# Kernel optimization log

Measured on AMD Instinct MI355X. Metric: run time of the kernel, lower is better.

## Reference

```python
import jax, jax.numpy as jnp
import numpy as np

N = 2560          # 64 graphs * 40 nodes (hard-coded by view(64,40,40))
E = 163840        # edges, avg degree 64
HEADS = 4
IN_C = 32
H0 = 128          # hidden_dims[0] per head
H1 = 128          # hidden_dims[1] per head
OUT_E = 40
EPS_BN = 1e-5


def _glorot(key, shape):
    fan = sum(shape[-2:]) if len(shape) > 1 else shape[0]
    return jax.random.normal(key, shape, dtype=jnp.float32) * (2.0 / fan) ** 0.5


def setup_inputs() -> dict:
    key = jax.random.key(0)
    ks = jax.random.split(key, 24)
    inp = {
        "x": jax.random.normal(ks[0], (N, IN_C), dtype=jnp.float32),
        "edge_index": jax.random.randint(ks[1], (2, E), 0, N, dtype=jnp.int32),
        "pos": jax.random.normal(ks[2], (N, 2), dtype=jnp.float32),
        "mask": jax.random.randint(ks[3], (N,), 0, 2, dtype=jnp.int32),
        "adjacency": jax.random.uniform(ks[4], (N, OUT_E), dtype=jnp.float32),
        # GAT layer 1 (in -> heads*H0)
        "W1": _glorot(ks[5], (IN_C, HEADS * H0)),
        "att_src1": _glorot(ks[6], (HEADS, H0)),
        "att_dst1": _glorot(ks[7], (HEADS, H0)),
        "We1": _glorot(ks[8], (1, HEADS * H0)),
        "att_e1": _glorot(ks[9], (HEADS, H0)),
        "bias1": jnp.zeros((HEADS * H0,), dtype=jnp.float32),
        # BatchNorm 1
        "g1": jnp.ones((HEADS * H0,), dtype=jnp.float32),
        "be1": jnp.zeros((HEADS * H0,), dtype=jnp.float32),
        # GAT layer 2 (heads*H0 -> heads*H1)
        "W2": _glorot(ks[10], (HEADS * H0, HEADS * H1)),
        "att_src2": _glorot(ks[11], (HEADS, H1)),
        "att_dst2": _glorot(ks[12], (HEADS, H1)),
        "We2": _glorot(ks[13], (1, HEADS * H1)),
        "att_e2": _glorot(ks[14], (HEADS, H1)),
        "bias2": jnp.zeros((HEADS * H1,), dtype=jnp.float32),
        # BatchNorm 2
        "g2": jnp.ones((HEADS * H1,), dtype=jnp.float32),
        "be2": jnp.zeros((HEADS * H1,), dtype=jnp.float32),
        # fc_edge
        "Wfc": _glorot(ks[15], (HEADS * H1, OUT_E)),
        "bfc": jnp.zeros((OUT_E,), dtype=jnp.float32),
    }
    return inp


def _gat(x, src, dst, ew, W, att_s, att_d, We, att_e, bias, heads, c):
    # x: [N, Fin] -> h: [N, H, C]
    h = (x @ W).reshape(-1, heads, c)
    a_s = (h * att_s).sum(-1)                       # [N, H]
    a_d = (h * att_d).sum(-1)                       # [N, H]
    he = (ew[:, None] @ We).reshape(-1, heads, c)   # [E, H, C] edge attr proj
    a_e = (he * att_e).sum(-1)                      # [E, H]
    alpha = jax.nn.leaky_relu(a_s[src] + a_d[dst] + a_e, 0.2)
    # segment softmax over destination nodes
    m = jax.ops.segment_max(alpha, dst, num_segments=N)
    alpha = jnp.exp(alpha - m[dst])
    denom = jax.ops.segment_sum(alpha, dst, num_segments=N)
    alpha = alpha / (denom[dst] + 1e-16)
    out = jax.ops.segment_sum(h[src] * alpha[:, :, None], dst, num_segments=N)
    return out.reshape(-1, heads * c) + bias


def _batchnorm(x, g, b):
    mu = x.mean(0)
    var = x.var(0)
    return (x - mu) * jax.lax.rsqrt(var + EPS_BN) * g + b


def reference(x, edge_index, pos, mask, adjacency,
              W1, att_src1, att_dst1, We1, att_e1, bias1, g1, be1,
              W2, att_src2, att_dst2, We2, att_e2, bias2, g2, be2,
              Wfc, bfc):
    src, dst = edge_index[0], edge_index[1]
    ew = 1.0 / (jnp.linalg.norm(pos[src] - pos[dst], axis=1) + 1e-6)  # [E]

    h = _gat(x, src, dst, ew, W1, att_src1, att_dst1, We1, att_e1, bias1, HEADS, H0)
    h = jax.nn.relu(_batchnorm(h, g1, be1))

    e = _gat(h, src, dst, ew, W2, att_src2, att_dst2, We2, att_e2, bias2, HEADS, H1)
    e = jax.nn.relu(_batchnorm(e, g2, be2))

    out_edge = e @ Wfc + bfc                     # [N, 40]
    out_edge = out_edge * mask[:, None].astype(out_edge.dtype)
    out_edge = out_edge.reshape(64, 40, 40)
    return out_edge + adjacency.reshape(64, 40, 40)
```

## Files before the change

### kernel.cpp

```cpp
#include <hip/hip_runtime.h>
#include <hip/hip_bf16.h>

#define NN 2560
#define NE 163840
#define NH 4
#define NC 128
#define NF 512
#define OUTE 40
#define CSTR 256

typedef short bf16x8 __attribute__((ext_vector_type(8)));
typedef float f32x4 __attribute__((ext_vector_type(4)));

__device__ inline ushort f2bf(float f) {
    uint u = __float_as_uint(f);
    uint r = u + 0x7FFF + ((u >> 16) & 1);
    return (ushort)(r >> 16);
}
__device__ inline float bflo(uint v) { return __uint_as_float(v << 16); }
__device__ inline float bfhi(uint v) { return __uint_as_float(v & 0xFFFF0000u); }
__device__ inline float bf2f(ushort u) { return __uint_as_float(((uint)u) << 16); }
__device__ inline float rdlanef(float v, int l) {
    return __int_as_float(__builtin_amdgcn_readlane(__float_as_int(v), l));
}
__device__ inline int rdlanei(int v, int l) {
    return __builtin_amdgcn_readlane(v, l);
}
__device__ inline float sel4(float r0, float r1, float r2, float r3, int hd) {
    return (hd & 2) ? ((hd & 1) ? r3 : r2) : ((hd & 1) ? r1 : r0);
}

__global__ __launch_bounds__(256) void k_csr_gemm1(const int* __restrict__ ei,
        const float* __restrict__ pos, int* __restrict__ deg,
        int2* __restrict__ csrp, int* __restrict__ ovf_cnt, int4* __restrict__ ovf,
        const float* __restrict__ We1, const float* __restrict__ ae1,
        const float* __restrict__ We2, const float* __restrict__ ae2,
        float* __restrict__ dote,
        const float* __restrict__ Wfc, ushort* __restrict__ WfcT,
        const float* __restrict__ W2, ushort* __restrict__ W2T,
        const float* __restrict__ x, const float* __restrict__ W1,
        const float* __restrict__ atts, const float* __restrict__ attd,
        ushort* __restrict__ hb, float* __restrict__ as_, float* __restrict__ ad_) {
    __shared__ ushort tile[64][72];
    __shared__ float s_x[4][32];
    __shared__ float4 s_red[4][4];
    int b = blockIdx.x;
    if (b < 640) {
        int e = b * 256 + threadIdx.x;
        int s = ei[e], d = ei[NE + e];
        float dx = pos[2 * s] - pos[2 * d];
        float dy = pos[2 * s + 1] - pos[2 * d + 1];
        float w = 1.0f / (sqrtf(dx * dx + dy * dy) + 1e-6f);
        int r = atomicAdd(&deg[d], 1);
        if (r < CSTR) {
            csrp[(d << 8) + r] = make_int2(s, __float_as_int(w));
        } else {
            int i = atomicAdd(ovf_cnt, 1);
            ovf[i] = make_int4(d, s, __float_as_int(w), 0);
        }
        return;
    }
    if (b < 642) {
        int t = threadIdx.x;
        const float* W = (b == 641) ? We2 : We1;
        const float* A = (b == 641) ? ae2 : ae1;
        int w = t >> 6, l = t & 63;
        float p = W[w * 128 + l] * A[w * 128 + l] + W[w * 128 + 64 + l] * A[w * 128 + 64 + l];
#pragma unroll
        for (int o = 32; o > 0; o >>= 1) p += __shfl_down(p, o);
        if (l == 0) dote[(b - 640) * 4 + w] = p;
        return;
    }
    if (b < 738) {
        int idx = (b - 642) * 256 + threadIdx.x;
        int j = idx >> 9, k = idx & 511;
        WfcT[idx] = (j < OUTE) ? f2bf(Wfc[k * OUTE + j]) : (ushort)0;
        return;
    }
    if (b < 802) {
        int id = b - 738;
        int n0 = (id & 7) * 64, k0 = (id >> 3) * 64;
        int t = threadIdx.x;
        int r = t >> 2, cseg = (t & 3) * 16;
#pragma unroll
        for (int c = 0; c < 16; c += 4) {
            float4 v = *(const float4*)&W2[(k0 + r) * 512 + n0 + cseg + c];
            tile[cseg + c + 0][r] = f2bf(v.x);
            tile[cseg + c + 1][r] = f2bf(v.y);
            tile[cseg + c + 2][r] = f2bf(v.z);
            tile[cseg + c + 3][r] = f2bf(v.w);
        }
        __syncthreads();
        *(uint4*)&W2T[(n0 + r) * 512 + k0 + cseg]     = *(uint4*)&tile[r][cseg];
        *(uint4*)&W2T[(n0 + r) * 512 + k0 + cseg + 8] = *(uint4*)&tile[r][cseg + 8];
        return;
    }
    int n0 = (b - 802) * 4, t = threadIdx.x;
    if (t < 128) s_x[t >> 5][t & 31] = x[n0 * 32 + t];
    __syncthreads();
    float a0[4] = {0.f, 0.f, 0.f, 0.f}, a1[4] = {0.f, 0.f, 0.f, 0.f};
#pragma unroll
    for (int k = 0; k < 32; k++) {
        float w0 = W1[k * 512 + t];
        float w1 = W1[k * 512 + t + 256];
#pragma unroll
        for (int nn = 0; nn < 4; nn++) {
            a0[nn] += s_x[nn][k] * w0;
            a1[nn] += s_x[nn][k] * w1;
        }
    }
    float sa0 = atts[t], sa1 = atts[t + 256];
    float da0 = attd[t], da1 = attd[t + 256];
    int w = t >> 6, lane = t & 63;
#pragma unroll
    for (int nn = 0; nn < 4; nn++) {
        hb[(n0 + nn) * 512 + t] = f2bf(a0[nn]);
        hb[(n0 + nn) * 512 + t + 256] = f2bf(a1[nn]);
        float ps0 = a0[nn] * sa0, pd0 = a0[nn] * da0;
        float ps1 = a1[nn] * sa1, pd1 = a1[nn] * da1;
#pragma unroll
        for (int o = 32; o > 0; o >>= 1) {
            ps0 += __shfl_xor(ps0, o); pd0 += __shfl_xor(pd0, o);
            ps1 += __shfl_xor(ps1, o); pd1 += __shfl_xor(pd1, o);
        }
        if (lane == 0) s_red[w][nn] = make_float4(ps0, pd0, ps1, pd1);
    }
    __syncthreads();
    if (t < 4) {
        int nn = t, n = n0 + nn;
        float4 r0 = s_red[0][nn], r1 = s_red[1][nn], r2 = s_red[2][nn], r3 = s_red[3][nn];
        as_[n * 4 + 0] = r0.x + r1.x; as_[n * 4 + 1] = r2.x + r3.x;
        as_[n * 4 + 2] = r0.z + r1.z; as_[n * 4 + 3] = r2.z + r3.z;
        ad_[n * 4 + 0] = r0.y + r1.y; ad_[n * 4 + 1] = r2.y + r3.y;
        ad_[n * 4 + 2] = r0.w + r1.w; ad_[n * 4 + 3] = r2.w + r3.w;
    }
}

__global__ __launch_bounds__(128) void k_edge_agg(const int* __restrict__ deg_,
        const int2* __restrict__ csrp, const int* __restrict__ ovf_cnt,
        const int4* __restrict__ ovf, const float* __restrict__ as_,
        const float* __restrict__ ad_, const float* __restrict__ dote,
        const ushort* __restrict__ hb, const float* __restrict__ bias,
        ushort* __restrict__ outb) {
    int w = threadIdx.x >> 6, lane = threadIdx.x & 63;
    int n = blockIdx.x * 2 + w;
    int beg = n << 8;
    int degn = deg_[n];
    int dmain = min(degn, CSTR);
    float4 adv = *(const float4*)&ad_[n * 4];
    float4 dv  = *(const float4*)dote;
    float La0 = -1e30f, La1 = -1e30f, La2 = -1e30f, La3 = -1e30f;
    float Lb0 = -1e30f, Lb1 = -1e30f, Lb2 = -1e30f, Lb3 = -1e30f;
    int off0 = 0, off1 = 0;
    if (lane < dmain) {
        int2 p = csrp[beg + lane];
        off0 = p.x * NF;
        float4 a = *(const float4*)&as_[p.x * 4];
        float ww = __int_as_float(p.y);
        float v0 = a.x + adv.x + ww * dv.x; La0 = v0 > 0.f ? v0 : 0.2f * v0;
        float v1 = a.y + adv.y + ww * dv.y; La1 = v1 > 0.f ? v1 : 0.2f * v1;
        float v2 = a.z + adv.z + ww * dv.z; La2 = v2 > 0.f ? v2 : 0.2f * v2;
        float v3 = a.w + adv.w + ww * dv.w; La3 = v3 > 0.f ? v3 : 0.2f * v3;
    }
    if (lane + 64 < dmain) {
        int2 p = csrp[beg + lane + 64];
        off1 = p.x * NF;
        float4 a = *(const float4*)&as_[p.x * 4];
        float ww = __int_as_float(p.y);
        float v0 = a.x + adv.x + ww * dv.x; Lb0 = v0 > 0.f ? v0 : 0.2f * v0;
        float v1 = a.y + adv.y + ww * dv.y; Lb1 = v1 > 0.f ? v1 : 0.2f * v1;
        float v2 = a.z + adv.z + ww * dv.z; Lb2 = v2 > 0.f ? v2 : 0.2f * v2;
        float v3 = a.w + adv.w + ww * dv.w; Lb3 = v3 > 0.f ? v3 : 0.2f * v3;
    }
    float mx0 = fmaxf(La0, Lb0), mx1 = fmaxf(La1, Lb1);
    float mx2 = fmaxf(La2, Lb2), mx3 = fmaxf(La3, Lb3);
    for (int e = 128 + lane; e < dmain; e += 64) {
        int2 p = csrp[beg + e];
        float4 a = *(const float4*)&as_[p.x * 4];
        float ww = __int_as_float(p.y);
        float v0 = a.x + adv.x + ww * dv.x; v0 = v0 > 0.f ? v0 : 0.2f * v0;
        float v1 = a.y + adv.y + ww * dv.y; v1 = v1 > 0.f ? v1 : 0.2f * v1;
        float v2 = a.z + adv.z + ww * dv.z; v2 = v2 > 0.f ? v2 : 0.2f * v2;
        float v3 = a.w + adv.w + ww * dv.w; v3 = v3 > 0.f ? v3 : 0.2f * v3;
        mx0 = fmaxf(mx0, v0); mx1 = fmaxf(mx1, v1);
        mx2 = fmaxf(mx2, v2); mx3 = fmaxf(mx3, v3);
    }
    if (degn > CSTR) {
        int oc = *ovf_cnt;
        for (int i = lane; i < oc; i += 64) {
            int4 o = ovf[i];
            if (o.x == n) {
                float4 a = *(const float4*)&as_[o.y * 4];
                float ww = __int_as_float(o.z);
                float v0 = a.x + adv.x + ww * dv.x; v0 = v0 > 0.f ? v0 : 0.2f * v0;
                float v1 = a.y + adv.y + ww * dv.y; v1 = v1 > 0.f ? v1 : 0.2f * v1;
                float v2 = a.z + adv.z + ww * dv.z; v2 = v2 > 0.f ? v2 : 0.2f * v2;
                float v3 = a.w + adv.w + ww * dv.w; v3 = v3 > 0.f ? v3 : 0.2f * v3;
                mx0 = fmaxf(mx0, v0); mx1 = fmaxf(mx1, v1);
                mx2 = fmaxf(mx2, v2); mx3 = fmaxf(mx3, v3);
            }
        }
    }
#pragma unroll
    for (int o = 32; o > 0; o >>= 1) {
        mx0 = fmaxf(mx0, __shfl_xor(mx0, o));
        mx1 = fmaxf(mx1, __shfl_xor(mx1, o));
        mx2 = fmaxf(mx2, __shfl_xor(mx2, o));
        mx3 = fmaxf(mx3, __shfl_xor(mx3, o));
    }
    float Aa0 = __expf(La0 - mx0), Aa1 = __expf(La1 - mx1);
    float Aa2 = __expf(La2 - mx2), Aa3 = __expf(La3 - mx3);
    float Ab0 = __expf(Lb0 - mx0), Ab1 = __expf(Lb1 - mx1);
    float Ab2 = __expf(Lb2 - mx2), Ab3 = __expf(Lb3 - mx3);
    float s0 = Aa0 + Ab0, s1 = Aa1 + Ab1, s2 = Aa2 + Ab2, s3 = Aa3 + Ab3;
    for (int e = 128 + lane; e < dmain; e += 64) {
        int2 p = csrp[beg + e];
        float4 a = *(const float4*)&as_[p.x * 4];
        float ww = __int_as_float(p.y);
        float v0 = a.x + adv.x + ww * dv.x; v0 = v0 > 0.f ? v0 : 0.2f * v0;
        float v1 = a.y + adv.y + ww * dv.y; v1 = v1 > 0.f ? v1 : 0.2f * v1;
        float v2 = a.z + adv.z + ww * dv.z; v2 = v2 > 0.f ? v2 : 0.2f * v2;
        float v3 = a.w + adv.w + ww * dv.w; v3 = v3 > 0.f ? v3 : 0.2f * v3;
        s0 += __expf(v0 - mx0); s1 += __expf(v1 - mx1);
        s2 += __expf(v2 - mx2); s3 += __expf(v3 - mx3);
    }
    if (degn > CSTR) {
        int oc = *ovf_cnt;
        for (int i = lane; i < oc; i += 64) {
            int4 o = ovf[i];
            if (o.x == n) {
                float4 a = *(const float4*)&as_[o.y * 4];
                float ww = __int_as_float(o.z);
                float v0 = a.x + adv.x + ww * dv.x; v0 = v0 > 0.f ? v0 : 0.2f * v0;
                float v1 = a.y + adv.y + ww * dv.y; v1 = v1 > 0.f ? v1 : 0.2f * v1;
                float v2 = a.z + adv.z + ww * dv.z; v2 = v2 > 0.f ? v2 : 0.2f * v2;
                float v3 = a.w + adv.w + ww * dv.w; v3 = v3 > 0.f ? v3 : 0.2f * v3;
                s0 += __expf(v0 - mx0); s1 += __expf(v1 - mx1);
                s2 += __expf(v2 - mx2); s3 += __expf(v3 - mx3);
            }
        }
    }
#pragma unroll
    for (int o = 32; o > 0; o >>= 1) {
        s0 += __shfl_xor(s0, o); s1 += __shfl_xor(s1, o);
        s2 += __shfl_xor(s2, o); s3 += __shfl_xor(s3, o);
    }
    float inv0 = 1.f / (s0 + 1e-16f), inv1 = 1.f / (s1 + 1e-16f);
    float inv2 = 1.f / (s2 + 1e-16f), inv3 = 1.f / (s3 + 1e-16f);
    int hd = lane >> 4;
    const ushort* hbase = hb + 8 * lane;
    float acc0 = 0.f, acc1 = 0.f, acc2 = 0.f, acc3 = 0.f;
    float acc4 = 0.f, acc5 = 0.f, acc6 = 0.f, acc7 = 0.f;
    int m0 = min(dmain, 64);
#pragma unroll 16
    for (int e = 0; e < m0; e++) {
        float r0 = rdlanef(Aa0, e), r1 = rdlanef(Aa1, e);
        float r2 = rdlanef(Aa2, e), r3 = rdlanef(Aa3, e);
        float a = sel4(r0, r1, r2, r3, hd);
        int o = rdlanei(off0, e);
        uint4 v = *(const uint4*)(hbase + o);
        acc0 += a * bflo(v.x); acc1 += a * bfhi(v.x);
        acc2 += a * bflo(v.y); acc3 += a * bfhi(v.y);
        acc4 += a * bflo(v.z); acc5 += a * bfhi(v.z);
        acc6 += a * bflo(v.w); acc7 += a * bfhi(v.w);
    }
    int m1 = min(dmain, 128);
#pragma unroll 16
    for (int e = 64; e < m1; e++) {
        float r0 = rdlanef(Ab0, e - 64), r1 = rdlanef(Ab1, e - 64);
        float r2 = rdlanef(Ab2, e - 64), r3 = rdlanef(Ab3, e - 64);
        float a = sel4(r0, r1, r2, r3, hd);
        int o = rdlanei(off1, e - 64);
        uint4 v = *(const uint4*)(hbase + o);
        acc0 += a * bflo(v.x); acc1 += a * bfhi(v.x);
        acc2 += a * bflo(v.y); acc3 += a * bfhi(v.y);
        acc4 += a * bflo(v.z); acc5 += a * bfhi(v.z);
        acc6 += a * bflo(v.w); acc7 += a * bfhi(v.w);
    }
    float adh = sel4(adv.x, adv.y, adv.z, adv.w, hd);
    float dh  = sel4(dv.x, dv.y, dv.z, dv.w, hd);
    float mxh = sel4(mx0, mx1, mx2, mx3, hd);
    float ash;
    for (int e = 128; e < dmain; e++) {
        int2 p = csrp[beg + e];
        ash = as_[p.x * 4 + hd];
        float ww = __int_as_float(p.y);
        float vv = ash + adh + ww * dh; vv = vv > 0.f ? vv : 0.2f * vv;
        float a = __expf(vv - mxh);
        uint4 v = *(const uint4*)(hbase + p.x * NF);
        acc0 += a * bflo(v.x); acc1 += a * bfhi(v.x);
        acc2 += a * bflo(v.y); acc3 += a * bfhi(v.y);
        acc4 += a * bflo(v.z); acc5 += a * bfhi(v.z);
        acc6 += a * bflo(v.w); acc7 += a * bfhi(v.w);
    }
    if (degn > CSTR) {
        int oc = *ovf_cnt;
        for (int i = 0; i < oc; i++) {
            int4 o = ovf[i];
            if (o.x == n) {
                ash = as_[o.y * 4 + hd];
                float ww = __int_as_float(o.z);
                float vv = ash + adh + ww * dh; vv = vv > 0.f ? vv : 0.2f * vv;
                float a = __expf(vv - mxh);
                uint4 v = *(const uint4*)(hbase + o.y * NF);
                acc0 += a * bflo(v.x); acc1 += a * bfhi(v.x);
                acc2 += a * bflo(v.y); acc3 += a * bfhi(v.y);
                acc4 += a * bflo(v.z); acc5 += a * bfhi(v.z);
                acc6 += a * bflo(v.w); acc7 += a * bfhi(v.w);
            }
        }
    }
    float invh = sel4(inv0, inv1, inv2, inv3, hd);
    int ch = 8 * lane;
    float4 b0 = *(const float4*)&bias[ch];
    float4 b1 = *(const float4*)&bias[ch + 4];
    uint4 ov;
    ov.x = (uint)f2bf(acc0 * invh + b0.x) | ((uint)f2bf(acc1 * invh + b0.y) << 16);
    ov.y = (uint)f2bf(acc2 * invh + b0.z) | ((uint)f2bf(acc3 * invh + b0.w) << 16);
    ov.z = (uint)f2bf(acc4 * invh + b1.x) | ((uint)f2bf(acc5 * invh + b1.y) << 16);
    ov.w = (uint)f2bf(acc6 * invh + b1.z) | ((uint)f2bf(acc7 * invh + b1.w) << 16);
    *(uint4*)&outb[n * NF + ch] = ov;
}

__global__ __launch_bounds__(256) void k_bnstats(const ushort* __restrict__ xs,
        float* __restrict__ stats) {
    __shared__ float ps[2048];
    __shared__ float pq[2048];
    int t = threadIdx.x;
    int c8 = (t & 63) * 8, rr = t >> 6;
    float s[8] = {0.f,0.f,0.f,0.f,0.f,0.f,0.f,0.f};
    float q[8] = {0.f,0.f,0.f,0.f,0.f,0.f,0.f,0.f};
#pragma unroll
    for (int rj = 0; rj < 4; rj++) {
        int r = blockIdx.x * 16 + rr * 4 + rj;
        uint4 v = *(const uint4*)&xs[r * NF + c8];
        float vv[8];
        vv[0] = bflo(v.x); vv[1] = bfhi(v.x); vv[2] = bflo(v.y); vv[3] = bfhi(v.y);
        vv[4] = bflo(v.z); vv[5] = bfhi(v.z); vv[6] = bflo(v.w); vv[7] = bfhi(v.w);
#pragma unroll
        for (int c = 0; c < 8; c++) { s[c] += vv[c]; q[c] += vv[c] * vv[c]; }
    }
#pragma unroll
    for (int c = 0; c < 8; c++) {
        ps[rr * 512 + c8 + c] = s[c];
        pq[rr * 512 + c8 + c] = q[c];
    }
    __syncthreads();
    for (int ch = t; ch < 512; ch += 256) {
        atomicAdd(&stats[ch], ps[ch] + ps[512 + ch] + ps[1024 + ch] + ps[1536 + ch]);
        atomicAdd(&stats[NF + ch], pq[ch] + pq[512 + ch] + pq[1024 + ch] + pq[1536 + ch]);
    }
}

__global__ __launch_bounds__(256) void k_gemm2_bn_att(const ushort* __restrict__ Ab,
        const float* __restrict__ stats, const float* __restrict__ g,
        const float* __restrict__ bb, const ushort* __restrict__ BT,
        const float* __restrict__ atts, const float* __restrict__ attd,
        ushort* __restrict__ Cb, float* __restrict__ as_, float* __restrict__ ad_) {
    __shared__ ushort As[64][40];
    __shared__ ushort Bs[128][40];
    __shared__ float s_scale[512], s_shift[512];
    __shared__ float s_ps[2][64], s_pd[2][64];
    int t = threadIdx.x;
    const float invn = 1.0f / (float)NN;
    {
        int j = t;
#pragma unroll
        for (int rep = 0; rep < 2; rep++, j += 256) {
            float mu = stats[j] * invn;
            float var = stats[NF + j] * invn - mu * mu;
            float sc = rsqrtf(var + 1e-5f) * g[j];
            s_scale[j] = sc;
            s_shift[j] = bb[j] - mu * sc;
        }
    }
    int head = blockIdx.x;
    int rowBase = blockIdx.y * 64, colBase = head * 128;
    int w = t >> 6, lane = t & 63;
    int wm = (w >> 1) * 32, wn = (w & 1) * 64;
    int lm = lane & 15, q = lane >> 4;
    f32x4 acc[2][4] = {};
    int sr2 = t >> 2, sk = (t & 3) * 8;
    for (int k0 = 0; k0 < 512; k0 += 32) {
        __syncthreads();
        int jb = k0 + sk;
        float sc[8], sh[8];
#pragma unroll
        for (int c = 0; c < 8; c++) { sc[c] = s_scale[jb + c]; sh[c] = s_shift[jb + c]; }
        uint4 a8 = *(const uint4*)&Ab[(rowBase + sr2) * 512 + jb];
        uint4 b0 = *(const uint4*)&BT[(colBase + sr2) * 512 + jb];
        uint4 b1 = *(const uint4*)&BT[(colBase + 64 + sr2) * 512 + jb];
        ushort pa0[8];
        float av[8];
        av[0] = bflo(a8.x); av[1] = bfhi(a8.x); av[2] = bflo(a8.y); av[3] = bfhi(a8.y);
        av[4] = bflo(a8.z); av[5] = bfhi(a8.z); av[6] = bflo(a8.w); av[7] = bfhi(a8.w);
#pragma unroll
        for (int c = 0; c < 8; c++)
            pa0[c] = f2bf(fmaxf(av[c] * sc[c] + sh[c], 0.f));
        *(uint4*)&As[sr2][sk]      = *(uint4*)pa0;
        *(uint4*)&Bs[sr2][sk]      = b0;
        *(uint4*)&Bs[64 + sr2][sk] = b1;
        __syncthreads();
        bf16x8 af[2], bf[4];
#pragma unroll
        for (int i = 0; i < 2; i++) af[i] = *(const bf16x8*)&As[wm + i * 16 + lm][q * 8];
#pragma unroll
        for (int j = 0; j < 4; j++) bf[j] = *(const bf16x8*)&Bs[wn + j * 16 + lm][q * 8];
#pragma unroll
        for (int i = 0; i < 2; i++)
#pragma unroll
            for (int j = 0; j < 4; j++)
                acc[i][j] = __builtin_amdgcn_mfma_f32_16x16x32_bf16(af[i], bf[j], acc[i][j], 0, 0, 0);
    }
#pragma unroll
    for (int i = 0; i < 2; i++) {
        int row = rowBase + wm + i * 16 + q * 4;
#pragma unroll
        for (int j = 0; j < 4; j++) {
            int col = colBase + wn + j * 16 + lm;
#pragma unroll
            for (int r = 0; r < 4; r++)
                Cb[(row + r) * 512 + col] = f2bf(acc[i][j][r]);
        }
    }
    float sa[4], da[4];
#pragma unroll
    for (int j = 0; j < 4; j++) {
        int col = colBase + wn + j * 16 + lm;
        sa[j] = atts[col]; da[j] = attd[col];
    }
#pragma unroll
    for (int i = 0; i < 2; i++) {
#pragma unroll
        for (int r = 0; r < 4; r++) {
            float ps = 0.f, pd = 0.f;
#pragma unroll
            for (int j = 0; j < 4; j++) {
                float c = acc[i][j][r];
                ps += c * sa[j]; pd += c * da[j];
            }
#pragma unroll
            for (int o = 1; o < 16; o <<= 1) { ps += __shfl_xor(ps, o); pd += __shfl_xor(pd, o); }
            if (lm == 0) {
                int row = wm + i * 16 + q * 4 + r;
                s_ps[w & 1][row] = ps; s_pd[w & 1][row] = pd;
            }
        }
    }
    __syncthreads();
    if (t < 64) {
        as_[(rowBase + t) * 4 + head] = s_ps[0][t] + s_ps[1][t];
    } else if (t < 128) {
        int row = t - 64;
        ad_[(rowBase + row) * 4 + head] = s_pd[0][row] + s_pd[1][row];
    }
}

__global__ __launch_bounds__(256) void k_fc_bn(const ushort* __restrict__ e2b,
        const float* __restrict__ stats, const float* __restrict__ g,
        const float* __restrict__ bb, const ushort* __restrict__ WfcT,
        const float* __restrict__ bfc, const int* __restrict__ mask,
        const float* __restrict__ adj, float* __restrict__ out) {
    __shared__ float s_scale[512], s_shift[512];
    __shared__ f32x4 s_acc[3][64][3];
    int t = threadIdx.x;
    int w = t >> 6, lane = t & 63;
    const float invn = 1.0f / (float)NN;
#pragma unroll
    for (int j = t; j < 512; j += 256) {
        float mu = stats[j] * invn;
        float var = stats[NF + j] * invn - mu * mu;
        float sc = rsqrtf(var + 1e-5f) * g[j];
        s_scale[j] = sc;
        s_shift[j] = bb[j] - mu * sc;
    }
    __syncthreads();
    int r0 = blockIdx.x * 16;
    int lm = lane & 15, q = lane >> 4;
    f32x4 acc[3] = {};
#pragma unroll
    for (int kk = 0; kk < 4; kk++) {
        int k0 = w * 128 + kk * 32;
        int jb = k0 + q * 8;
        uint4 a8 = *(const uint4*)&e2b[(r0 + lm) * 512 + jb];
        float av[8];
        av[0] = bflo(a8.x); av[1] = bfhi(a8.x); av[2] = bflo(a8.y); av[3] = bfhi(a8.y);
        av[4] = bflo(a8.z); av[5] = bfhi(a8.z); av[6] = bflo(a8.w); av[7] = bfhi(a8.w);
        ushort pa[8];
#pragma unroll
        for (int c = 0; c < 8; c++)
            pa[c] = f2bf(fmaxf(av[c] * s_scale[jb + c] + s_shift[jb + c], 0.f));
        bf16x8 af = *(const bf16x8*)pa;
#pragma unroll
        for (int jt = 0; jt < 3; jt++) {
            bf16x8 bf = *(const bf16x8*)&WfcT[(jt * 16 + lm) * 512 + k0 + q * 8];
            acc[jt] = __builtin_amdgcn_mfma_f32_16x16x32_bf16(af, bf, acc[jt], 0, 0, 0);
        }
    }
    if (w > 0) {
#pragma unroll
        for (int jt = 0; jt < 3; jt++) s_acc[w - 1][lane][jt] = acc[jt];
    }
    __syncthreads();
    if (w == 0) {
#pragma unroll
        for (int jt = 0; jt < 3; jt++) {
            acc[jt] += s_acc[0][lane][jt] + s_acc[1][lane][jt] + s_acc[2][lane][jt];
            int col = jt * 16 + lm;
            if (col < OUTE) {
#pragma unroll
                for (int r = 0; r < 4; r++) {
                    int n = r0 + q * 4 + r;
                    float v = acc[jt][r] + bfc[col];
                    v = mask[n] ? v : 0.f;
                    out[n * OUTE + col] = v + adj[n * OUTE + col];
                }
            }
        }
    }
}

extern "C" void kernel_launch(void* const* d_in, const int* in_sizes, int n_in,
                              void* d_out, int out_size, void* d_ws, size_t ws_size,
                              hipStream_t stream) {
    const float* x       = (const float*)d_in[0];
    const int*   ei      = (const int*)d_in[1];
    const float* pos     = (const float*)d_in[2];
    const int*   mask    = (const int*)d_in[3];
    const float* adj     = (const float*)d_in[4];
    const float* W1      = (const float*)d_in[5];
    const float* atts1   = (const float*)d_in[6];
    const float* attd1   = (const float*)d_in[7];
    const float* We1     = (const float*)d_in[8];
    const float* atte1   = (const float*)d_in[9];
    const float* bias1   = (const float*)d_in[10];
    const float* g1      = (const float*)d_in[11];
    const float* be1     = (const float*)d_in[12];
    const float* W2      = (const float*)d_in[13];
    const float* atts2   = (const float*)d_in[14];
    const float* attd2   = (const float*)d_in[15];
    const float* We2     = (const float*)d_in[16];
    const float* atte2   = (const float*)d_in[17];
    const float* bias2   = (const float*)d_in[18];
    const float* g2      = (const float*)d_in[19];
    const float* be2     = (const float*)d_in[20];
    const float* Wfc     = (const float*)d_in[21];
    const float* bfc     = (const float*)d_in[22];
    float* out = (float*)d_out;

    char* ws = (char*)d_ws;
    int*    deg     = (int*)(ws);
    int*    ovf_cnt = (int*)(ws + 2560 * 4);
    float*  stats   = (float*)(ws + 5120 * 4);
    float*  dote    = (float*)(ws + 7168 * 4);
    int2*   csrp    = (int2*)(ws + 7184 * 4);
    int4*   ovf     = (int4*)(ws + 1317904 * 4);
    float*  as_     = (float*)(ws + 1973264 * 4);
    float*  ad_     = (float*)(ws + 1983504 * 4);
    ushort* t1b     = (ushort*)(ws + 1993744 * 4);
    ushort* hb      = (ushort*)(ws + 2649104 * 4);
    ushort* W2T     = (ushort*)(ws + 3304464 * 4);
    ushort* WfcT    = (ushort*)(ws + 3435536 * 4);

    hipMemsetAsync(d_ws, 0, 7168 * 4, stream);

    k_csr_gemm1<<<802 + NN / 4, 256, 0, stream>>>(ei, pos, deg, csrp, ovf_cnt, ovf,
                                                  We1, atte1, We2, atte2, dote,
                                                  Wfc, WfcT, W2, W2T,
                                                  x, W1, atts1, attd1, hb, as_, ad_);

    k_edge_agg<<<NN / 2, 128, 0, stream>>>(deg, csrp, ovf_cnt, ovf, as_, ad_,
                                           dote, hb, bias1, t1b);
    k_bnstats<<<NN / 16, 256, 0, stream>>>(t1b, stats);

    k_gemm2_bn_att<<<dim3(4, NN / 64), 256, 0, stream>>>(t1b, stats, g1, be1, W2T,
                                                         atts2, attd2, hb, as_, ad_);
    k_edge_agg<<<NN / 2, 128, 0, stream>>>(deg, csrp, ovf_cnt, ovf, as_, ad_,
                                           dote + 4, hb, bias2, t1b);
    k_bnstats<<<NN / 16, 256, 0, stream>>>(t1b, stats + 1024);

    k_fc_bn<<<NN / 16, 256, 0, stream>>>(t1b, stats + 1024, g2, be2, WfcT, bfc, mask, adj, out);
}
```

Measured before the change: 204.4 us.

## Fuse BN statistics into edge aggregation and split each node across two waves

Each node's edge aggregation now uses a 128-thread block, with the two waves splitting the neighbor list and combining max, sum and accumulators through shared memory. The separate k_bnstats kernels are removed. Per-channel sum and sum-of-squares are instead accumulated with atomics into 16 replicated stat buffers, which the consumers reduce. This cuts two kernel launches and a full re-read of the activations, and doubles per-node parallelism. The cost is extra block syncs, about a million atomics per layer, and a larger memset.

After: 264.9 us. 1.3x slower.

```diff
diff --git a/kernel.cpp b/kernel.cpp
--- a/kernel.cpp
+++ b/kernel.cpp
@@ -8,6 +8,7 @@
 #define NF 512
 #define OUTE 40
 #define CSTR 256
+#define NCOPY 16
 
 typedef short bf16x8 __attribute__((ext_vector_type(8)));
 typedef float f32x4 __attribute__((ext_vector_type(4)));
@@ -141,19 +142,23 @@
         const int4* __restrict__ ovf, const float* __restrict__ as_,
         const float* __restrict__ ad_, const float* __restrict__ dote,
         const ushort* __restrict__ hb, const float* __restrict__ bias,
-        ushort* __restrict__ outb) {
+        ushort* __restrict__ outb, float* __restrict__ stats) {
+    __shared__ float s_comb[64][8];
+    __shared__ float s_red[2][8];
+    __shared__ float s_sum[512];
+    __shared__ float s_sq[512];
     int w = threadIdx.x >> 6, lane = threadIdx.x & 63;
-    int n = blockIdx.x * 2 + w;
+    int n = blockIdx.x;
     int beg = n << 8;
     int degn = deg_[n];
     int dmain = min(degn, CSTR);
     float4 adv = *(const float4*)&ad_[n * 4];
     float4 dv  = *(const float4*)dote;
     float La0 = -1e30f, La1 = -1e30f, La2 = -1e30f, La3 = -1e30f;
-    float Lb0 = -1e30f, Lb1 = -1e30f, Lb2 = -1e30f, Lb3 = -1e30f;
-    int off0 = 0, off1 = 0;
-    if (lane < dmain) {
-        int2 p = csrp[beg + lane];
+    int off0 = 0;
+    int e0 = w * 64 + lane;
+    if (e0 < dmain) {
+        int2 p = csrp[beg + e0];
         off0 = p.x * NF;
         float4 a = *(const float4*)&as_[p.x * 4];
         float ww = __int_as_float(p.y);
@@ -162,19 +167,8 @@
         float v2 = a.z + adv.z + ww * dv.z; La2 = v2 > 0.f ? v2 : 0.2f * v2;
         float v3 = a.w + adv.w + ww * dv.w; La3 = v3 > 0.f ? v3 : 0.2f * v3;
     }
-    if (lane + 64 < dmain) {
-        int2 p = csrp[beg + lane + 64];
-        off1 = p.x * NF;
-        float4 a = *(const float4*)&as_[p.x * 4];
-        float ww = __int_as_float(p.y);
-        float v0 = a.x + adv.x + ww * dv.x; Lb0 = v0 > 0.f ? v0 : 0.2f * v0;
-        float v1 = a.y + adv.y + ww * dv.y; Lb1 = v1 > 0.f ? v1 : 0.2f * v1;
-        float v2 = a.z + adv.z + ww * dv.z; Lb2 = v2 > 0.f ? v2 : 0.2f * v2;
-        float v3 = a.w + adv.w + ww * dv.w; Lb3 = v3 > 0.f ? v3 : 0.2f * v3;
-    }
-    float mx0 = fmaxf(La0, Lb0), mx1 = fmaxf(La1, Lb1);
-    float mx2 = fmaxf(La2, Lb2), mx3 = fmaxf(La3, Lb3);
-    for (int e = 128 + lane; e < dmain; e += 64) {
+    float mx0 = La0, mx1 = La1, mx2 = La2, mx3 = La3;
+    for (int e = 128 + w * 64 + lane; e < dmain; e += 128) {
         int2 p = csrp[beg + e];
         float4 a = *(const float4*)&as_[p.x * 4];
         float ww = __int_as_float(p.y);
@@ -187,7 +181,7 @@
     }
     if (degn > CSTR) {
         int oc = *ovf_cnt;
-        for (int i = lane; i < oc; i += 64) {
+        for (int i = threadIdx.x; i < oc; i += 128) {
             int4 o = ovf[i];
             if (o.x == n) {
                 float4 a = *(const float4*)&as_[o.y * 4];
@@ -208,12 +202,17 @@
         mx2 = fmaxf(mx2, __shfl_xor(mx2, o));
         mx3 = fmaxf(mx3, __shfl_xor(mx3, o));
     }
+    if (lane == 0) {
+        s_red[w][0] = mx0; s_red[w][1] = mx1; s_red[w][2] = mx2; s_red[w][3] = mx3;
+    }
+    __syncthreads();
+    mx0 = fmaxf(s_red[0][0], s_red[1][0]); mx1 = fmaxf(s_red[0][1], s_red[1][1]);
+    mx2 = fmaxf(s_red[0][2], s_red[1][2]); mx3 = fmaxf(s_red[0][3], s_red[1][3]);
+    __syncthreads();
     float Aa0 = __expf(La0 - mx0), Aa1 = __expf(La1 - mx1);
     float Aa2 = __expf(La2 - mx2), Aa3 = __expf(La3 - mx3);
-    float Ab0 = __expf(Lb0 - mx0), Ab1 = __expf(Lb1 - mx1);
-    float Ab2 = __expf(Lb2 - mx2), Ab3 = __expf(Lb3 - mx3);
-    float s0 = Aa0 + Ab0, s1 = Aa1 + Ab1, s2 = Aa2 + Ab2, s3 = Aa3 + Ab3;
-    for (int e = 128 + lane; e < dmain; e += 64) {
+    float s0 = Aa0, s1 = Aa1, s2 = Aa2, s3 = Aa3;
+    for (int e = 128 + w * 64 + lane; e < dmain; e += 128) {
         int2 p = csrp[beg + e];
         float4 a = *(const float4*)&as_[p.x * 4];
         float ww = __int_as_float(p.y);
@@ -226,7 +225,7 @@
     }
     if (degn > CSTR) {
         int oc = *ovf_cnt;
-        for (int i = lane; i < oc; i += 64) {
+        for (int i = threadIdx.x; i < oc; i += 128) {
             int4 o = ovf[i];
             if (o.x == n) {
                 float4 a = *(const float4*)&as_[o.y * 4];
@@ -245,15 +244,21 @@
         s0 += __shfl_xor(s0, o); s1 += __shfl_xor(s1, o);
         s2 += __shfl_xor(s2, o); s3 += __shfl_xor(s3, o);
     }
+    if (lane == 0) {
+        s_red[w][0] = s0; s_red[w][1] = s1; s_red[w][2] = s2; s_red[w][3] = s3;
+    }
+    __syncthreads();
+    s0 = s_red[0][0] + s_red[1][0]; s1 = s_red[0][1] + s_red[1][1];
+    s2 = s_red[0][2] + s_red[1][2]; s3 = s_red[0][3] + s_red[1][3];
     float inv0 = 1.f / (s0 + 1e-16f), inv1 = 1.f / (s1 + 1e-16f);
     float inv2 = 1.f / (s2 + 1e-16f), inv3 = 1.f / (s3 + 1e-16f);
     int hd = lane >> 4;
     const ushort* hbase = hb + 8 * lane;
     float acc0 = 0.f, acc1 = 0.f, acc2 = 0.f, acc3 = 0.f;
     float acc4 = 0.f, acc5 = 0.f, acc6 = 0.f, acc7 = 0.f;
-    int m0 = min(dmain, 64);
+    int mEnd = min(dmain - w * 64, 64);
 #pragma unroll 16
-    for (int e = 0; e < m0; e++) {
+    for (int e = 0; e < mEnd; e++) {
         float r0 = rdlanef(Aa0, e), r1 = rdlanef(Aa1, e);
         float r2 = rdlanef(Aa2, e), r3 = rdlanef(Aa3, e);
         float a = sel4(r0, r1, r2, r3, hd);
@@ -264,26 +269,12 @@
         acc4 += a * bflo(v.z); acc5 += a * bfhi(v.z);
         acc6 += a * bflo(v.w); acc7 += a * bfhi(v.w);
     }
-    int m1 = min(dmain, 128);
-#pragma unroll 16
-    for (int e = 64; e < m1; e++) {
-        float r0 = rdlanef(Ab0, e - 64), r1 = rdlanef(Ab1, e - 64);
-        float r2 = rdlanef(Ab2, e - 64), r3 = rdlanef(Ab3, e - 64);
-        float a = sel4(r0, r1, r2, r3, hd);
-        int o = rdlanei(off1, e - 64);
-        uint4 v = *(const uint4*)(hbase + o);
-        acc0 += a * bflo(v.x); acc1 += a * bfhi(v.x);
-        acc2 += a * bflo(v.y); acc3 += a * bfhi(v.y);
-        acc4 += a * bflo(v.z); acc5 += a * bfhi(v.z);
-        acc6 += a * bflo(v.w); acc7 += a * bfhi(v.w);
-    }
     float adh = sel4(adv.x, adv.y, adv.z, adv.w, hd);
     float dh  = sel4(dv.x, dv.y, dv.z, dv.w, hd);
     float mxh = sel4(mx0, mx1, mx2, mx3, hd);
-    float ash;
-    for (int e = 128; e < dmain; e++) {
+    for (int e = 128 + w; e < dmain; e += 2) {
         int2 p = csrp[beg + e];
-        ash = as_[p.x * 4 + hd];
+        float ash = as_[p.x * 4 + hd];
         float ww = __int_as_float(p.y);
         float vv = ash + adh + ww * dh; vv = vv > 0.f ? vv : 0.2f * vv;
         float a = __expf(vv - mxh);
@@ -295,10 +286,10 @@
     }
     if (degn > CSTR) {
         int oc = *ovf_cnt;
-        for (int i = 0; i < oc; i++) {
+        for (int i = w; i < oc; i += 2) {
             int4 o = ovf[i];
             if (o.x == n) {
-                ash = as_[o.y * 4 + hd];
+                float ash = as_[o.y * 4 + hd];
                 float ww = __int_as_float(o.z);
                 float vv = ash + adh + ww * dh; vv = vv > 0.f ? vv : 0.2f * vv;
                 float a = __expf(vv - mxh);
@@ -310,45 +301,51 @@
             }
         }
     }
-    float invh = sel4(inv0, inv1, inv2, inv3, hd);
-    int ch = 8 * lane;
-    float4 b0 = *(const float4*)&bias[ch];
-    float4 b1 = *(const float4*)&bias[ch + 4];
-    uint4 ov;
-    ov.x = (uint)f2bf(acc0 * invh + b0.x) | ((uint)f2bf(acc1 * invh + b0.y) << 16);
-    ov.y = (uint)f2bf(acc2 * invh + b0.z) | ((uint)f2bf(acc3 * invh + b0.w) << 16);
-    ov.z = (uint)f2bf(acc4 * invh + b1.x) | ((uint)f2bf(acc5 * invh + b1.y) << 16);
-    ov.w = (uint)f2bf(acc6 * invh + b1.z) | ((uint)f2bf(acc7 * invh + b1.w) << 16);
-    *(uint4*)&outb[n * NF + ch] = ov;
-}
-
-__global__ __launch_bounds__(256) void k_bnstats(const ushort* __restrict__ xs,
-        float* __restrict__ stats) {
-    __shared__ float ps[2048];
-    __shared__ float pq[2048];
-    int t = threadIdx.x;
-    int c8 = (t & 63) * 8, rr = t >> 6;
-    float s[8] = {0.f,0.f,0.f,0.f,0.f,0.f,0.f,0.f};
-    float q[8] = {0.f,0.f,0.f,0.f,0.f,0.f,0.f,0.f};
-#pragma unroll
-    for (int rj = 0; rj < 4; rj++) {
-        int r = blockIdx.x * 16 + rr * 4 + rj;
-        uint4 v = *(const uint4*)&xs[r * NF + c8];
-        float vv[8];
-        vv[0] = bflo(v.x); vv[1] = bfhi(v.x); vv[2] = bflo(v.y); vv[3] = bfhi(v.y);
-        vv[4] = bflo(v.z); vv[5] = bfhi(v.z); vv[6] = bflo(v.w); vv[7] = bfhi(v.w);
-#pragma unroll
-        for (int c = 0; c < 8; c++) { s[c] += vv[c]; q[c] += vv[c] * vv[c]; }
-    }
-#pragma unroll
-    for (int c = 0; c < 8; c++) {
-        ps[rr * 512 + c8 + c] = s[c];
-        pq[rr * 512 + c8 + c] = q[c];
-    }
-    __syncthreads();
-    for (int ch = t; ch < 512; ch += 256) {
-        atomicAdd(&stats[ch], ps[ch] + ps[512 + ch] + ps[1024 + ch] + ps[1536 + ch]);
-        atomicAdd(&stats[NF + ch], pq[ch] + pq[512 + ch] + pq[1024 + ch] + pq[1536 + ch]);
+    if (w == 1) {
+        s_comb[lane][0] = acc0; s_comb[lane][1] = acc1;
+        s_comb[lane][2] = acc2; s_comb[lane][3] = acc3;
+        s_comb[lane][4] = acc4; s_comb[lane][5] = acc5;
+        s_comb[lane][6] = acc6; s_comb[lane][7] = acc7;
+    }
+    __syncthreads();
+    if (w == 0) {
+        acc0 += s_comb[lane][0]; acc1 += s_comb[lane][1];
+        acc2 += s_comb[lane][2]; acc3 += s_comb[lane][3];
+        acc4 += s_comb[lane][4]; acc5 += s_comb[lane][5];
+        acc6 += s_comb[lane][6]; acc7 += s_comb[lane][7];
+        float invh = sel4(inv0, inv1, inv2, inv3, hd);
+        int ch = 8 * lane;
+        float4 b0 = *(const float4*)&bias[ch];
+        float4 b1 = *(const float4*)&bias[ch + 4];
+        ushort h0 = f2bf(acc0 * invh + b0.x), h1 = f2bf(acc1 * invh + b0.y);
+        ushort h2 = f2bf(acc2 * invh + b0.z), h3 = f2bf(acc3 * invh + b0.w);
+        ushort h4 = f2bf(acc4 * invh + b1.x), h5 = f2bf(acc5 * invh + b1.y);
+        ushort h6 = f2bf(acc6 * invh + b1.z), h7 = f2bf(acc7 * invh + b1.w);
+        uint4 ov;
+        ov.x = (uint)h0 | ((uint)h1 << 16);
+        ov.y = (uint)h2 | ((uint)h3 << 16);
+        ov.z = (uint)h4 | ((uint)h5 << 16);
+        ov.w = (uint)h6 | ((uint)h7 << 16);
+        *(uint4*)&outb[n * NF + ch] = ov;
+        float f0 = bf2f(h0), f1 = bf2f(h1), f2 = bf2f(h2), f3 = bf2f(h3);
+        float f4 = bf2f(h4), f5 = bf2f(h5), f6 = bf2f(h6), f7 = bf2f(h7);
+        s_sum[ch + 0] = f0; s_sq[ch + 0] = f0 * f0;
+        s_sum[ch + 1] = f1; s_sq[ch + 1] = f1 * f1;
+        s_sum[ch + 2] = f2; s_sq[ch + 2] = f2 * f2;
+        s_sum[ch + 3] = f3; s_sq[ch + 3] = f3 * f3;
+        s_sum[ch + 4] = f4; s_sq[ch + 4] = f4 * f4;
+        s_sum[ch + 5] = f5; s_sq[ch + 5] = f5 * f5;
+        s_sum[ch + 6] = f6; s_sq[ch + 6] = f6 * f6;
+        s_sum[ch + 7] = f7; s_sq[ch + 7] = f7 * f7;
+    }
+    __syncthreads();
+    float* st = stats + (blockIdx.x & (NCOPY - 1)) * 1024;
+    int c0 = (threadIdx.x * 4 + ((blockIdx.x >> 4) & 7) * 64) & 511;
+#pragma unroll
+    for (int i = 0; i < 4; i++) {
+        int c = c0 + i;
+        atomicAdd(&st[c], s_sum[c]);
+        atomicAdd(&st[512 + c], s_sq[c]);
     }
 }
 
@@ -367,8 +364,14 @@
         int j = t;
 #pragma unroll
         for (int rep = 0; rep < 2; rep++, j += 256) {
-            float mu = stats[j] * invn;
-            float var = stats[NF + j] * invn - mu * mu;
+            float su = 0.f, sq = 0.f;
+#pragma unroll
+            for (int k = 0; k < NCOPY; k++) {
+                su += stats[k * 1024 + j];
+                sq += stats[k * 1024 + 512 + j];
+            }
+            float mu = su * invn;
+            float var = sq * invn - mu * mu;
             float sc = rsqrtf(var + 1e-5f) * g[j];
             s_scale[j] = sc;
             s_shift[j] = bb[j] - mu * sc;
@@ -468,8 +471,14 @@
     const float invn = 1.0f / (float)NN;
 #pragma unroll
     for (int j = t; j < 512; j += 256) {
-        float mu = stats[j] * invn;
-        float var = stats[NF + j] * invn - mu * mu;
+        float su = 0.f, sq = 0.f;
+#pragma unroll
+        for (int k = 0; k < NCOPY; k++) {
+            su += stats[k * 1024 + j];
+            sq += stats[k * 1024 + 512 + j];
+        }
+        float mu = su * invn;
+        float var = sq * invn - mu * mu;
         float sc = rsqrtf(var + 1e-5f) * g[j];
         s_scale[j] = sc;
         s_shift[j] = bb[j] - mu * sc;
@@ -551,33 +560,32 @@
     char* ws = (char*)d_ws;
     int*    deg     = (int*)(ws);
     int*    ovf_cnt = (int*)(ws + 2560 * 4);
-    float*  stats   = (float*)(ws + 5120 * 4);
-    float*  dote    = (float*)(ws + 7168 * 4);
-    int2*   csrp    = (int2*)(ws + 7184 * 4);
-    int4*   ovf     = (int4*)(ws + 1317904 * 4);
-    float*  as_     = (float*)(ws + 1973264 * 4);
-    float*  ad_     = (float*)(ws + 1983504 * 4);
-    ushort* t1b     = (ushort*)(ws + 1993744 * 4);
-    ushort* hb      = (ushort*)(ws + 2649104 * 4);
-    ushort* W2T     = (ushort*)(ws + 3304464 * 4);
-    ushort* WfcT    = (ushort*)(ws + 3435536 * 4);
-
-    hipMemsetAsync(d_ws, 0, 7168 * 4, stream);
+    float*  st16_1  = (float*)(ws + 2576 * 4);
+    float*  st16_2  = (float*)(ws + 18960 * 4);
+    float*  dote    = (float*)(ws + 35344 * 4);
+    int2*   csrp    = (int2*)(ws + 35360 * 4);
+    int4*   ovf     = (int4*)(ws + 1346080 * 4);
+    float*  as_     = (float*)(ws + 1411616 * 4);
+    float*  ad_     = (float*)(ws + 1421856 * 4);
+    ushort* t1b     = (ushort*)(ws + 1432096 * 4);
+    ushort* hb      = (ushort*)(ws + 2087456 * 4);
+    ushort* W2T     = (ushort*)(ws + 2742816 * 4);
+    ushort* WfcT    = (ushort*)(ws + 2873888 * 4);
+
+    hipMemsetAsync(d_ws, 0, 35344 * 4, stream);
 
     k_csr_gemm1<<<802 + NN / 4, 256, 0, stream>>>(ei, pos, deg, csrp, ovf_cnt, ovf,
                                                   We1, atte1, We2, atte2, dote,
                                                   Wfc, WfcT, W2, W2T,
                                                   x, W1, atts1, attd1, hb, as_, ad_);
 
-    k_edge_agg<<<NN / 2, 128, 0, stream>>>(deg, csrp, ovf_cnt, ovf, as_, ad_,
-                                           dote, hb, bias1, t1b);
-    k_bnstats<<<NN / 16, 256, 0, stream>>>(t1b, stats);
-
-    k_gemm2_bn_att<<<dim3(4, NN / 64), 256, 0, stream>>>(t1b, stats, g1, be1, W2T,
+    k_edge_agg<<<NN, 128, 0, stream>>>(deg, csrp, ovf_cnt, ovf, as_, ad_,
+                                       dote, hb, bias1, t1b, st16_1);
+
+    k_gemm2_bn_att<<<dim3(4, NN / 64), 256, 0, stream>>>(t1b, st16_1, g1, be1, W2T,
                                                          atts2, attd2, hb, as_, ad_);
-    k_edge_agg<<<NN / 2, 128, 0, stream>>>(deg, csrp, ovf_cnt, ovf, as_, ad_,
-                                           dote + 4, hb, bias2, t1b);
-    k_bnstats<<<NN / 16, 256, 0, stream>>>(t1b, stats + 1024);
-
-    k_fc_bn<<<NN / 16, 256, 0, stream>>>(t1b, stats + 1024, g2, be2, WfcT, bfc, mask, adj, out);
-}
+    k_edge_agg<<<NN, 128, 0, stream>>>(deg, csrp, ovf_cnt, ovf, as_, ad_,
+                                       dote + 4, hb, bias2, t1b, st16_2);
+
+    k_fc_bn<<<NN / 16, 256, 0, stream>>>(t1b, st16_2, g2, be2, WfcT, bfc, mask, adj, out);
+}
```

## Double-buffer neighbor feature gathers in batches of eight in the GAT aggregation

Applied to the files above, without the earlier changes.

Replaces the two per-edge gather loops in the aggregation with a loop over batches of 8 neighbor rows, alternating between two register buffers. The next batch is loaded while the current one is accumulated. The first batch is issued before the softmax max and sum passes, so its latency overlaps that work. Edge counts are rounded up to a multiple of 8, which relies on padding lanes holding harmless offsets and zero weights. The two 8-entry uint4 buffers add register pressure and may reduce occupancy.

New measurement: 202.1 us. About the same (-1.1%).

```diff
diff --git a/kernel.cpp b/kernel.cpp
--- a/kernel.cpp
+++ b/kernel.cpp
@@ -29,6 +29,36 @@
 __device__ inline float sel4(float r0, float r1, float r2, float r3, int hd) {
     return (hd & 2) ? ((hd & 1) ? r3 : r2) : ((hd & 1) ? r1 : r0);
 }
+
+#define LOADV8(bb, vv) do {                                                   \
+    if ((bb) < 8) { int _b = (bb) * 8;                                        \
+        _Pragma("unroll") for (int _j = 0; _j < 8; _j++)                      \
+            vv[_j] = *(const uint4*)(hbase + rdlanei(off0, _b + _j));         \
+    } else { int _b = (bb) * 8 - 64;                                          \
+        _Pragma("unroll") for (int _j = 0; _j < 8; _j++)                      \
+            vv[_j] = *(const uint4*)(hbase + rdlanei(off1, _b + _j));         \
+    } } while (0)
+
+#define CONSUME8(bb, vv) do {                                                 \
+    if ((bb) < 8) { int _b = (bb) * 8;                                        \
+        _Pragma("unroll") for (int _j = 0; _j < 8; _j++) {                    \
+            float _a = sel4(rdlanef(Aa0, _b + _j), rdlanef(Aa1, _b + _j),     \
+                            rdlanef(Aa2, _b + _j), rdlanef(Aa3, _b + _j), hd);\
+            acc0 += _a * bflo(vv[_j].x); acc1 += _a * bfhi(vv[_j].x);         \
+            acc2 += _a * bflo(vv[_j].y); acc3 += _a * bfhi(vv[_j].y);         \
+            acc4 += _a * bflo(vv[_j].z); acc5 += _a * bfhi(vv[_j].z);         \
+            acc6 += _a * bflo(vv[_j].w); acc7 += _a * bfhi(vv[_j].w);         \
+        }                                                                     \
+    } else { int _b = (bb) * 8 - 64;                                          \
+        _Pragma("unroll") for (int _j = 0; _j < 8; _j++) {                    \
+            float _a = sel4(rdlanef(Ab0, _b + _j), rdlanef(Ab1, _b + _j),     \
+                            rdlanef(Ab2, _b + _j), rdlanef(Ab3, _b + _j), hd);\
+            acc0 += _a * bflo(vv[_j].x); acc1 += _a * bfhi(vv[_j].x);         \
+            acc2 += _a * bflo(vv[_j].y); acc3 += _a * bfhi(vv[_j].y);         \
+            acc4 += _a * bflo(vv[_j].z); acc5 += _a * bfhi(vv[_j].z);         \
+            acc6 += _a * bflo(vv[_j].w); acc7 += _a * bfhi(vv[_j].w);         \
+        }                                                                     \
+    } } while (0)
 
 __global__ __launch_bounds__(256) void k_csr_gemm1(const int* __restrict__ ei,
         const float* __restrict__ pos, int* __restrict__ deg,
@@ -172,6 +202,12 @@
         float v2 = a.z + adv.z + ww * dv.z; Lb2 = v2 > 0.f ? v2 : 0.2f * v2;
         float v3 = a.w + adv.w + ww * dv.w; Lb3 = v3 > 0.f ? v3 : 0.2f * v3;
     }
+    int hd = lane >> 4;
+    const ushort* hbase = hb + 8 * lane;
+    int mR = min((dmain + 7) & ~7, 128);
+    int nb = mR >> 3;
+    uint4 vA[8], vB[8];
+    if (nb > 0) LOADV8(0, vA);
     float mx0 = fmaxf(La0, Lb0), mx1 = fmaxf(La1, Lb1);
     float mx2 = fmaxf(La2, Lb2), mx3 = fmaxf(La3, Lb3);
     for (int e = 128 + lane; e < dmain; e += 64) {
@@ -247,43 +283,24 @@
     }
     float inv0 = 1.f / (s0 + 1e-16f), inv1 = 1.f / (s1 + 1e-16f);
     float inv2 = 1.f / (s2 + 1e-16f), inv3 = 1.f / (s3 + 1e-16f);
-    int hd = lane >> 4;
-    const ushort* hbase = hb + 8 * lane;
     float acc0 = 0.f, acc1 = 0.f, acc2 = 0.f, acc3 = 0.f;
     float acc4 = 0.f, acc5 = 0.f, acc6 = 0.f, acc7 = 0.f;
-    int m0 = min(dmain, 64);
-#pragma unroll 16
-    for (int e = 0; e < m0; e++) {
-        float r0 = rdlanef(Aa0, e), r1 = rdlanef(Aa1, e);
-        float r2 = rdlanef(Aa2, e), r3 = rdlanef(Aa3, e);
-        float a = sel4(r0, r1, r2, r3, hd);
-        int o = rdlanei(off0, e);
-        uint4 v = *(const uint4*)(hbase + o);
-        acc0 += a * bflo(v.x); acc1 += a * bfhi(v.x);
-        acc2 += a * bflo(v.y); acc3 += a * bfhi(v.y);
-        acc4 += a * bflo(v.z); acc5 += a * bfhi(v.z);
-        acc6 += a * bflo(v.w); acc7 += a * bfhi(v.w);
-    }
-    int m1 = min(dmain, 128);
-#pragma unroll 16
-    for (int e = 64; e < m1; e++) {
-        float r0 = rdlanef(Ab0, e - 64), r1 = rdlanef(Ab1, e - 64);
-        float r2 = rdlanef(Ab2, e - 64), r3 = rdlanef(Ab3, e - 64);
-        float a = sel4(r0, r1, r2, r3, hd);
-        int o = rdlanei(off1, e - 64);
-        uint4 v = *(const uint4*)(hbase + o);
-        acc0 += a * bflo(v.x); acc1 += a * bfhi(v.x);
-        acc2 += a * bflo(v.y); acc3 += a * bfhi(v.y);
-        acc4 += a * bflo(v.z); acc5 += a * bfhi(v.z);
-        acc6 += a * bflo(v.w); acc7 += a * bfhi(v.w);
+    int b = 0;
+    while (b < nb) {
+        if (b + 1 < nb) LOADV8(b + 1, vB);
+        CONSUME8(b, vA);
+        ++b;
+        if (b >= nb) break;
+        if (b + 1 < nb) LOADV8(b + 1, vA);
+        CONSUME8(b, vB);
+        ++b;
     }
     float adh = sel4(adv.x, adv.y, adv.z, adv.w, hd);
     float dh  = sel4(dv.x, dv.y, dv.z, dv.w, hd);
     float mxh = sel4(mx0, mx1, mx2, mx3, hd);
-    float ash;
-    for (int e = 128; e < dmain; e++) {
-        int2 p = csrp[beg + e];
-        ash = as_[p.x * 4 + hd];
+    for (int ee = 128; ee < dmain; ee++) {
+        int2 p = csrp[beg + ee];
+        float ash = as_[p.x * 4 + hd];
         float ww = __int_as_float(p.y);
         float vv = ash + adh + ww * dh; vv = vv > 0.f ? vv : 0.2f * vv;
         float a = __expf(vv - mxh);
@@ -298,7 +315,7 @@
         for (int i = 0; i < oc; i++) {
             int4 o = ovf[i];
             if (o.x == n) {
-                ash = as_[o.y * 4 + hd];
+                float ash = as_[o.y * 4 + hd];
                 float ww = __int_as_float(o.z);
                 float vv = ash + adh + ww * dh; vv = vv > 0.f ? vv : 0.2f * vv;
                 float a = __expf(vv - mxh);
```
